# Performance work log

Measured on AMD Instinct MI355X. Metric: run time of the kernel, lower is better.

## Reference

```python
import jax, jax.numpy as jnp
import numpy as np

B, S, D, H, W = 4, 2048, 512, 8, 16
DK = D // H


def setup_inputs() -> dict:
    key = jax.random.key(0)
    ks = jax.random.split(key, 11)
    scale = 1.0 / np.sqrt(D)
    return {
        "query": jax.random.normal(ks[0], (B, S, D), jnp.float32),
        "key": jax.random.normal(ks[1], (B, S, D), jnp.float32),
        "value": jax.random.normal(ks[2], (B, S, D), jnp.float32),
        "Wq": jax.random.normal(ks[3], (D, D), jnp.float32) * scale,
        "bq": jnp.zeros((D,), jnp.float32),
        "Wk": jax.random.normal(ks[4], (D, D), jnp.float32) * scale,
        "bk": jnp.zeros((D,), jnp.float32),
        "Wv": jax.random.normal(ks[5], (D, D), jnp.float32) * scale,
        "bv": jnp.zeros((D,), jnp.float32),
        "Wo": jax.random.normal(ks[6], (D, D), jnp.float32) * scale,
        "bo": jnp.zeros((D,), jnp.float32),
    }


def reference(query, key, value, Wq, bq, Wk, bk, Wv, bv, Wo, bo):
    b, s, d = query.shape
    # QKV projections -> [b, H, s, DK]
    Q = (query @ Wq + bq).reshape(b, s, H, DK).transpose(0, 2, 1, 3)
    K = (key @ Wk + bk).reshape(b, s, H, DK).transpose(0, 2, 1, 3)
    V = (value @ Wv + bv).reshape(b, s, H, DK).transpose(0, 2, 1, 3)
    # Dense scores (faithful to original O(n^2) math), then static band mask
    scores = jnp.einsum("bhqd,bhkd->bhqk", Q, K) / jnp.sqrt(jnp.array(DK, scores_dtype := Q.dtype))
    idx = jnp.arange(s)
    local = jnp.abs(idx[:, None] - idx[None, :]) <= W  # [s, s] band
    mask_value = jnp.finfo(scores.dtype).min
    scores = jnp.where(local[None, None], scores, mask_value)
    attn = jax.nn.softmax(scores, axis=-1)
    ctx = jnp.einsum("bhqk,bhkd->bhqd", attn, V)
    ctx = ctx.transpose(0, 2, 1, 3).reshape(b, s, d)
    return ctx @ Wo + bo
```

## Files before the change

kernel.cpp:

```cpp
#include <hip/hip_runtime.h>

typedef __attribute__((ext_vector_type(8))) short bf16x8;
typedef __attribute__((ext_vector_type(4))) float f32x4;
typedef __attribute__((ext_vector_type(4))) unsigned int u32x4;
typedef __attribute__((ext_vector_type(8))) unsigned short bfu8;

#define BB 4
#define SS 2048
#define DD 512
#define HH 8
#define DKK 64
#define WWIN 16
#define MTOT (BB*SS)
#define MKE  ((long)MTOT*DD)
#define NKE  ((long)DD*DD)

__device__ __forceinline__ unsigned short f2bf(float f) {
  unsigned int u = __float_as_uint(f);
  u += 0x7fffu + ((u >> 16) & 1u);
  return (unsigned short)(u >> 16);
}
__device__ __forceinline__ float bf2f(unsigned short s) {
  return __uint_as_float(((unsigned int)s) << 16);
}

__device__ __forceinline__ void gload_lds16(const unsigned short* g, unsigned short* l) {
  __builtin_amdgcn_global_load_lds((const __attribute__((address_space(1))) void*)g,
                                   (__attribute__((address_space(3))) void*)l, 16, 0, 0);
}

__global__ __launch_bounds__(256) void convert_w(
    const float* __restrict__ Wq, const float* __restrict__ Wk,
    const float* __restrict__ Wv, const float* __restrict__ Wo,
    const float* __restrict__ bq, const float* __restrict__ bk, const float* __restrict__ bv,
    unsigned short* __restrict__ wt, float* __restrict__ bias_all)
{
  int bx = blockIdx.x;
  if (bx >= 256) {
    int idx = (bx - 256) * 256 + threadIdx.x;
    bias_all[idx] = idx < DD ? bq[idx] : (idx < 2*DD ? bk[idx-DD] : bv[idx-2*DD]);
    return;
  }
  int wm = bx >> 6;
  int tile = bx & 63;
  int tr = tile >> 3, tc = tile & 7;
  const float* src = wm==0 ? Wq : wm==1 ? Wk : wm==2 ? Wv : Wo;
  unsigned short* dst = wt + (long)wm*NKE;
  __shared__ float tl[64][65];
  int t = threadIdx.x;
  int cr = t >> 6;
  int cc = t & 63;
  for (int p = 0; p < 16; ++p) {
    int row = p*4 + cr;
    tl[row][cc] = src[(long)(tr*64+row)*DD + tc*64 + cc];
  }
  __syncthreads();
  for (int p = 0; p < 16; ++p) {
    int orow = p*4 + cr;
    dst[(long)(tc*64 + orow)*DD + tr*64 + cc] = f2bf(tl[cc][orow]);
  }
}

template<int OUT_BF16, int A_FP32>
__global__ __launch_bounds__(256, 2) void gemm_rowpanel(
    const void* __restrict__ a0, const void* __restrict__ a1, const void* __restrict__ a2,
    const unsigned short* __restrict__ Btbase, long bZ,
    const float* __restrict__ biasBase, long biasZ,
    void* __restrict__ outBase, long outZ,
    int N, int K)
{
  const int z = blockIdx.z;
  const void* Av = z==0 ? a0 : z==1 ? a1 : a2;
  const unsigned short* Bt = Btbase + (long)z*bZ;
  const float* bias = biasBase + (long)z*biasZ;

  const int tid = threadIdx.x, lane = tid & 63, w = tid >> 6;
  const int c = lane & 15, g = lane >> 4;
  const int m0 = blockIdx.x * 32;

  __shared__ unsigned short lA[32*64];
  __shared__ unsigned short lB[512*64];

  f32x4 acc[2][8] = {};

  for (int kt = 0; kt < K; kt += 64) {
    for (int i = 0; i < 16; ++i) {
      int u = i*256 + tid;
      int row = u >> 3, col = (u & 7) * 8;
      gload_lds16(Bt + (long)row*K + kt + col, &lB[i*2048 + w*512]);
    }
    {
      int row = tid >> 3, col = (tid & 7) * 8;
      if (A_FP32) {
        const float* Afp = (const float*)Av;
        const float* src = Afp + (long)(m0 + row)*K + kt + col;
        float4 f0 = *(const float4*)src;
        float4 f1 = *(const float4*)(src + 4);
        bfu8 o;
        o[0]=f2bf(f0.x); o[1]=f2bf(f0.y); o[2]=f2bf(f0.z); o[3]=f2bf(f0.w);
        o[4]=f2bf(f1.x); o[5]=f2bf(f1.y); o[6]=f2bf(f1.z); o[7]=f2bf(f1.w);
        *(bfu8*)&lA[tid*8] = o;
      } else {
        const unsigned short* A = (const unsigned short*)Av;
        gload_lds16(A + (long)(m0 + row)*K + kt + col, &lA[w*512]);
      }
    }
    __syncthreads();
    for (int kk = 0; kk < 2; ++kk) {
      bf16x8 af[2], bfr[8];
      for (int m = 0; m < 2; ++m)
        af[m] = *reinterpret_cast<const bf16x8*>(&lA[(m*16 + c)*64 + kk*32 + g*8]);
      for (int n = 0; n < 8; ++n)
        bfr[n] = *reinterpret_cast<const bf16x8*>(&lB[(w*128 + n*16 + c)*64 + kk*32 + g*8]);
      for (int m = 0; m < 2; ++m)
        for (int n = 0; n < 8; ++n)
          acc[m][n] = __builtin_amdgcn_mfma_f32_16x16x32_bf16(af[m], bfr[n], acc[m][n], 0, 0, 0);
    }
    __syncthreads();
  }

  for (int m = 0; m < 2; ++m) {
    int rbase = m0 + m*16 + g*4;
    for (int n = 0; n < 8; ++n) {
      int col = w*128 + n*16 + c;
      float bv = bias[col];
      for (int r = 0; r < 4; ++r) {
        float val = acc[m][n][r] + bv;
        long idx = (long)z*outZ + (long)(rbase + r)*N + col;
        if (OUT_BF16) ((unsigned short*)outBase)[idx] = f2bf(val);
        else          ((float*)outBase)[idx] = val;
      }
    }
  }
}

#define KP 76
#define PP 76
__global__ __launch_bounds__(256) void attn_kernel(
    const unsigned short* __restrict__ Qbf, const unsigned short* __restrict__ Kbf,
    const unsigned short* __restrict__ Vbf, unsigned short* __restrict__ ctxbf)
{
  const int q0 = blockIdx.x * 128;
  const int h  = blockIdx.y;
  const int b  = blockIdx.z;
  const int tid = threadIdx.x, lane = tid & 63, w = tid >> 6;
  const int c = lane & 15, g = lane >> 4;
  const int w0 = q0 - WWIN;

  __shared__ unsigned short K_l[160*KP];
  __shared__ unsigned short V_l[160*KP];
  __shared__ unsigned short P_l[4][32*PP];

  const long baseRow = (long)b*SS*DD + (long)h*DKK;
  const int qw0   = q0 + w*32;
  const int kbase = w*32;

  bf16x8 aq[2][2];
  for (int m = 0; m < 2; ++m)
    for (int kk = 0; kk < 2; ++kk)
      aq[m][kk] = *reinterpret_cast<const bf16x8*>(
          Qbf + baseRow + (long)(qw0 + m*16 + c)*DD + kk*32 + g*8);

  for (int i = 0; i < 5; ++i) {
    int u = i*256 + tid;
    int row = u >> 3, c8 = (u & 7) * 8;
    int gk = w0 + row;
    u32x4 kv = {0,0,0,0}, vv = {0,0,0,0};
    if (gk >= 0 && gk < SS) {
      kv = *(const u32x4*)(Kbf + baseRow + (long)gk*DD + c8);
      vv = *(const u32x4*)(Vbf + baseRow + (long)gk*DD + c8);
    }
    *(u32x4*)(&K_l[row*KP + c8]) = kv;
    *(u32x4*)(&V_l[row*KP + c8]) = vv;
  }
  __syncthreads();

  f32x4 accs[2][4] = {};
  __builtin_amdgcn_s_setprio(1);
  for (int kk = 0; kk < 2; ++kk) {
    bf16x8 bk[4];
    for (int n = 0; n < 4; ++n)
      bk[n] = *reinterpret_cast<const bf16x8*>(&K_l[(kbase + n*16 + c)*KP + kk*32 + g*8]);
    for (int m = 0; m < 2; ++m)
      for (int n = 0; n < 4; ++n)
        accs[m][n] = __builtin_amdgcn_mfma_f32_16x16x32_bf16(aq[m][kk], bk[n], accs[m][n], 0, 0, 0);
  }
  __builtin_amdgcn_s_setprio(0);

  float pden[2][4];
  for (int m = 0; m < 2; ++m) {
    for (int r = 0; r < 4; ++r) {
      int qi = m*16 + g*4 + r;
      float sv[4];
      float mx = -INFINITY;
      for (int n = 0; n < 4; ++n) {
        int kr = n*16 + c;
        int d  = kr - qi;
        int kg = w0 + kbase + kr;
        bool ok = (d >= 0) && (d <= 2*WWIN) && (kg >= 0) && (kg < SS);
        sv[n] = ok ? accs[m][n][r] * 0.125f : -INFINITY;
        mx = fmaxf(mx, sv[n]);
      }
      for (int off = 1; off < 16; off <<= 1) mx = fmaxf(mx, __shfl_xor(mx, off, 64));
      float sum = 0.f;
      for (int n = 0; n < 4; ++n) {
        float e = __expf(sv[n] - mx);
        sum += e;
        P_l[w][(m*16 + g*4 + r)*PP + n*16 + c] = f2bf(e);
      }
      for (int off = 1; off < 16; off <<= 1) sum += __shfl_xor(sum, off, 64);
      pden[m][r] = sum;
    }
  }
  __syncthreads();

  f32x4 acco[2][4] = {};
  for (int kk = 0; kk < 2; ++kk) {
    bf16x8 pa[2];
    for (int m = 0; m < 2; ++m)
      pa[m] = *reinterpret_cast<const bf16x8*>(&P_l[w][(m*16 + c)*PP + kk*32 + g*8]);
    bf16x8 bv[4];
    int kb = kbase + kk*32 + g*8;
    for (int n = 0; n < 4; ++n) {
      bfu8 t;
      for (int j = 0; j < 8; ++j) t[j] = V_l[(kb + j)*KP + n*16 + c];
      bv[n] = *reinterpret_cast<bf16x8*>(&t);
    }
    __builtin_amdgcn_s_setprio(1);
    for (int m = 0; m < 2; ++m)
      for (int n = 0; n < 4; ++n)
        acco[m][n] = __builtin_amdgcn_mfma_f32_16x16x32_bf16(pa[m], bv[n], acco[m][n], 0, 0, 0);
    __builtin_amdgcn_s_setprio(0);
  }

  for (int m = 0; m < 2; ++m) {
    for (int r = 0; r < 4; ++r) {
      int q = qw0 + m*16 + g*4 + r;
      float inv = 1.f / pden[m][r];
      for (int n = 0; n < 4; ++n)
        ctxbf[baseRow + (long)q*DD + n*16 + c] = f2bf(acco[m][n][r] * inv);
    }
  }
}

extern "C" void kernel_launch(void* const* d_in, const int* in_sizes, int n_in,
                              void* d_out, int out_size, void* d_ws, size_t ws_size,
                              hipStream_t stream) {
  const float* q  = (const float*)d_in[0];
  const float* k  = (const float*)d_in[1];
  const float* v  = (const float*)d_in[2];
  const float* Wq = (const float*)d_in[3];
  const float* bq = (const float*)d_in[4];
  const float* Wk = (const float*)d_in[5];
  const float* bk = (const float*)d_in[6];
  const float* Wv = (const float*)d_in[7];
  const float* bv = (const float*)d_in[8];
  const float* Wo = (const float*)d_in[9];
  const float* bo = (const float*)d_in[10];

  char* ws = (char*)d_ws;
  unsigned short* wtbf     = (unsigned short*)(ws);
  float*          bias_all = (float*)(ws + 2097152);
  unsigned short* qkvbf    = (unsigned short*)(ws + 2103296);
  unsigned short* ctxbf    = (unsigned short*)(ws + 27269120);

  convert_w<<<262, 256, 0, stream>>>(Wq, Wk, Wv, Wo, bq, bk, bv, wtbf, bias_all);
  gemm_rowpanel<1,1><<<dim3(MTOT/32, 1, 3), 256, 0, stream>>>(
      q, k, v, wtbf, NKE, bias_all, DD,
      (void*)qkvbf, MKE, DD, DD);
  attn_kernel<<<dim3(SS/128, HH, BB), 256, 0, stream>>>(
      qkvbf, qkvbf + MKE, qkvbf + 2*MKE, ctxbf);
  gemm_rowpanel<0,0><<<dim3(MTOT/32, 1, 1), 256, 0, stream>>>(
      ctxbf, ctxbf, ctxbf, wtbf + 3*NKE, 0, bo, 0,
      (void*)d_out, 0, DD, DD);
}
```

Before: 168.8 us.

## Rewrite projection GEMMs as 128x128 tiled, double-buffered, swizzled LDS kernels

Replaces the 32-row full-width panel GEMM with 128x128 output tiles and a 2x2 wave layout. LDS is double-buffered so the next K-tile's global loads overlap the MFMA work on the current one, and an XOR swizzle is meant to avoid LDS bank conflicts. Block IDs are remapped so that groups of blocks share A panels for L2 reuse, and s_setprio is raised around the MFMA bursts. The per-block accumulator footprint and LDS usage grow, which can cut occupancy, and fp32 A loads are now held in registers across the compute step.

```diff
diff --git a/kernel.cpp b/kernel.cpp
--- a/kernel.cpp
+++ b/kernel.cpp
@@ -62,70 +62,125 @@
 }
 
 template<int OUT_BF16, int A_FP32>
-__global__ __launch_bounds__(256, 2) void gemm_rowpanel(
+__global__ __launch_bounds__(256, 2) void gemm_dbuf(
     const void* __restrict__ a0, const void* __restrict__ a1, const void* __restrict__ a2,
     const unsigned short* __restrict__ Btbase, long bZ,
     const float* __restrict__ biasBase, long biasZ,
-    void* __restrict__ outBase, long outZ,
-    int N, int K)
+    void* __restrict__ outBase, long outZ, int N, int K)
 {
-  const int z = blockIdx.z;
+  const int bid   = blockIdx.x;
+  const int slot  = bid >> 3;
+  const int panel = (bid & 7) + 8 * (slot >> 2);
+  const int n0 = (slot & 3) * 128;
+  const int z  = panel >> 6;
+  const int m0 = (panel & 63) * 128;
+
   const void* Av = z==0 ? a0 : z==1 ? a1 : a2;
   const unsigned short* Bt = Btbase + (long)z*bZ;
   const float* bias = biasBase + (long)z*biasZ;
 
   const int tid = threadIdx.x, lane = tid & 63, w = tid >> 6;
+  const int wr = w >> 1, wc = w & 1;
   const int c = lane & 15, g = lane >> 4;
-  const int m0 = blockIdx.x * 32;
-
-  __shared__ unsigned short lA[32*64];
-  __shared__ unsigned short lB[512*64];
-
-  f32x4 acc[2][8] = {};
-
-  for (int kt = 0; kt < K; kt += 64) {
-    for (int i = 0; i < 16; ++i) {
+
+  __shared__ unsigned short lA[2][128*64];
+  __shared__ unsigned short lB[2][128*64];
+
+  f32x4 acc[4][4] = {};
+  float4 fa[8];
+  const int NT = K >> 6;
+
+  auto stageB = [&](int buf, int kt) {
+    #pragma unroll
+    for (int j = 0; j < 4; ++j) {
+      int u = w*256 + j*64 + lane;
+      int row = u >> 3, sl = (u & 7) ^ (row & 7);
+      gload_lds16(Bt + (long)(n0 + row)*K + kt + sl*8, &lB[buf][(w*256 + j*64)*8]);
+    }
+  };
+  auto stageA_lds = [&](int buf, int kt) {
+    const unsigned short* Ab = (const unsigned short*)Av;
+    #pragma unroll
+    for (int j = 0; j < 4; ++j) {
+      int u = w*256 + j*64 + lane;
+      int row = u >> 3, sl = (u & 7) ^ (row & 7);
+      gload_lds16(Ab + (long)(m0 + row)*K + kt + sl*8, &lA[buf][(w*256 + j*64)*8]);
+    }
+  };
+  auto loadA = [&](int kt) {
+    const float* Af = (const float*)Av;
+    #pragma unroll
+    for (int i = 0; i < 4; ++i) {
       int u = i*256 + tid;
       int row = u >> 3, col = (u & 7) * 8;
-      gload_lds16(Bt + (long)row*K + kt + col, &lB[i*2048 + w*512]);
-    }
-    {
-      int row = tid >> 3, col = (tid & 7) * 8;
-      if (A_FP32) {
-        const float* Afp = (const float*)Av;
-        const float* src = Afp + (long)(m0 + row)*K + kt + col;
-        float4 f0 = *(const float4*)src;
-        float4 f1 = *(const float4*)(src + 4);
-        bfu8 o;
-        o[0]=f2bf(f0.x); o[1]=f2bf(f0.y); o[2]=f2bf(f0.z); o[3]=f2bf(f0.w);
-        o[4]=f2bf(f1.x); o[5]=f2bf(f1.y); o[6]=f2bf(f1.z); o[7]=f2bf(f1.w);
-        *(bfu8*)&lA[tid*8] = o;
-      } else {
-        const unsigned short* A = (const unsigned short*)Av;
-        gload_lds16(A + (long)(m0 + row)*K + kt + col, &lA[w*512]);
-      }
-    }
+      const float* s = Af + (long)(m0 + row)*K + kt + col;
+      fa[2*i]   = *(const float4*)s;
+      fa[2*i+1] = *(const float4*)(s + 4);
+    }
+  };
+  auto writeA = [&](int buf) {
+    #pragma unroll
+    for (int i = 0; i < 4; ++i) {
+      int u = i*256 + tid;
+      int row = u >> 3, sl = u & 7;
+      bfu8 o;
+      o[0]=f2bf(fa[2*i].x);   o[1]=f2bf(fa[2*i].y);   o[2]=f2bf(fa[2*i].z);   o[3]=f2bf(fa[2*i].w);
+      o[4]=f2bf(fa[2*i+1].x); o[5]=f2bf(fa[2*i+1].y); o[6]=f2bf(fa[2*i+1].z); o[7]=f2bf(fa[2*i+1].w);
+      *(bfu8*)&lA[buf][row*64 + (sl ^ (row & 7))*8] = o;
+    }
+  };
+  auto compute = [&](int buf) {
+    #pragma unroll
+    for (int kk = 0; kk < 2; ++kk) {
+      bf16x8 af[4], bfr[4];
+      #pragma unroll
+      for (int m = 0; m < 4; ++m) {
+        int row = wr*64 + m*16 + c;
+        af[m] = *reinterpret_cast<const bf16x8*>(&lA[buf][row*64 + (((kk<<2)+g) ^ (row & 7))*8]);
+      }
+      #pragma unroll
+      for (int nn = 0; nn < 4; ++nn) {
+        int col = wc*64 + nn*16 + c;
+        bfr[nn] = *reinterpret_cast<const bf16x8*>(&lB[buf][col*64 + (((kk<<2)+g) ^ (col & 7))*8]);
+      }
+      __builtin_amdgcn_s_setprio(1);
+      #pragma unroll
+      for (int m = 0; m < 4; ++m)
+        #pragma unroll
+        for (int nn = 0; nn < 4; ++nn)
+          acc[m][nn] = __builtin_amdgcn_mfma_f32_16x16x32_bf16(af[m], bfr[nn], acc[m][nn], 0, 0, 0);
+      __builtin_amdgcn_s_setprio(0);
+    }
+  };
+
+  if (A_FP32) loadA(0); else stageA_lds(0, 0);
+  stageB(0, 0);
+  if (A_FP32) writeA(0);
+  __syncthreads();
+
+  int cur = 0;
+  for (int t = 0; t < NT; ++t) {
+    int nxt = cur ^ 1;
+    if (t + 1 < NT) {
+      if (A_FP32) loadA((t+1) << 6); else stageA_lds(nxt, (t+1) << 6);
+      stageB(nxt, (t+1) << 6);
+    }
+    compute(cur);
+    if (A_FP32 && t + 1 < NT) writeA(nxt);
     __syncthreads();
-    for (int kk = 0; kk < 2; ++kk) {
-      bf16x8 af[2], bfr[8];
-      for (int m = 0; m < 2; ++m)
-        af[m] = *reinterpret_cast<const bf16x8*>(&lA[(m*16 + c)*64 + kk*32 + g*8]);
-      for (int n = 0; n < 8; ++n)
-        bfr[n] = *reinterpret_cast<const bf16x8*>(&lB[(w*128 + n*16 + c)*64 + kk*32 + g*8]);
-      for (int m = 0; m < 2; ++m)
-        for (int n = 0; n < 8; ++n)
-          acc[m][n] = __builtin_amdgcn_mfma_f32_16x16x32_bf16(af[m], bfr[n], acc[m][n], 0, 0, 0);
-    }
-    __syncthreads();
-  }
-
-  for (int m = 0; m < 2; ++m) {
-    int rbase = m0 + m*16 + g*4;
-    for (int n = 0; n < 8; ++n) {
-      int col = w*128 + n*16 + c;
+    cur = nxt;
+  }
+
+  #pragma unroll
+  for (int m = 0; m < 4; ++m) {
+    int rbase = m0 + wr*64 + m*16 + g*4;
+    #pragma unroll
+    for (int nn = 0; nn < 4; ++nn) {
+      int col = n0 + wc*64 + nn*16 + c;
       float bv = bias[col];
+      #pragma unroll
       for (int r = 0; r < 4; ++r) {
-        float val = acc[m][n][r] + bv;
+        float val = acc[m][nn][r] + bv;
         long idx = (long)z*outZ + (long)(rbase + r)*N + col;
         if (OUT_BF16) ((unsigned short*)outBase)[idx] = f2bf(val);
         else          ((float*)outBase)[idx] = val;
@@ -265,12 +320,12 @@
   unsigned short* ctxbf    = (unsigned short*)(ws + 27269120);
 
   convert_w<<<262, 256, 0, stream>>>(Wq, Wk, Wv, Wo, bq, bk, bv, wtbf, bias_all);
-  gemm_rowpanel<1,1><<<dim3(MTOT/32, 1, 3), 256, 0, stream>>>(
+  gemm_dbuf<1,1><<<768, 256, 0, stream>>>(
       q, k, v, wtbf, NKE, bias_all, DD,
       (void*)qkvbf, MKE, DD, DD);
   attn_kernel<<<dim3(SS/128, HH, BB), 256, 0, stream>>>(
       qkvbf, qkvbf + MKE, qkvbf + 2*MKE, ctxbf);
-  gemm_rowpanel<0,0><<<dim3(MTOT/32, 1, 1), 256, 0, stream>>>(
+  gemm_dbuf<0,0><<<256, 256, 0, stream>>>(
       ctxbf, ctxbf, ctxbf, wtbf + 3*NKE, 0, bo, 0,
       (void*)d_out, 0, DD, DD);
 }
```

Result: faster. 158.4 us (-6.2%).
